# Kernel tuning notes

Hardware: AMD Instinct MI355X
Metric: run time of the kernel (lower is better)

Reference implementation:

```python
import jax, jax.numpy as jnp
import numpy as np

N = 120000   # current nodes
F = 256      # num_feat
H = 256      # num_hidden
L = 64       # num_logits
E_MP = 1000000  # message-passing edges
E = 200000      # scored edges
PREV = [60000, 80000, 100000]
PROX_WEIGHT = 0.3


def setup_inputs() -> dict:
    key = jax.random.key(0)
    ks = jax.random.split(key, 40)
    n = lambda k, shape, s=0.05: jax.random.normal(k, shape, dtype=jnp.float32) * s
    inp = {}
    inp["x"] = n(ks[0], (N, F), 1.0)
    inp["mp_adj"] = jax.random.randint(ks[1], (2, E_MP), 0, N)
    inp["edges"] = jax.random.randint(ks[2], (2, E), 0, N)
    inp["index"] = jax.random.randint(ks[3], (E,), 0, E)
    inp["prev_emb0"] = n(ks[4], (PREV[0], H), 1.0)
    inp["prev_emb1"] = n(ks[5], (PREV[1], H), 1.0)
    inp["prev_emb2"] = n(ks[6], (PREV[2], H), 1.0)
    # Module_L params
    inp["gc1_W"] = n(ks[7], (F, H))
    inp["gc1_b"] = jnp.zeros((H,), jnp.float32)
    inp["gc2_W"] = n(ks[8], (H, H))
    inp["gc2_b"] = jnp.zeros((H,), jnp.float32)
    inp["linear_W"] = n(ks[9], (2 * H, H))
    inp["linear_b"] = jnp.zeros((H,), jnp.float32)
    inp["weight_lin"] = n(ks[10], (H, H))
    inp["bias_lin"] = jnp.zeros((H,), jnp.float32)
    inp["w_q"] = n(ks[11], (H, H))
    inp["w_k"] = n(ks[12], (H, H))
    inp["w_v"] = n(ks[13], (H, H))
    # ensemble params
    inp["ml_w1"] = n(ks[14], (2 * H, H)); inp["ml_b1"] = jnp.zeros((H,), jnp.float32)
    inp["ml_w2"] = n(ks[15], (H, 1));     inp["ml_b2"] = jnp.zeros((1,), jnp.float32)
    inp["ms_w1"] = n(ks[16], (2 * H, H)); inp["ms_b1"] = jnp.zeros((H,), jnp.float32)
    inp["ms_w2"] = n(ks[17], (H, 1));     inp["ms_b2"] = jnp.zeros((1,), jnp.float32)
    inp["msdr_w"] = n(ks[18], (L, H));    inp["msdr_b"] = jnp.zeros((H,), jnp.float32)
    # Module_S logits and precomputed score tables
    inp["logits"] = n(ks[19], (N, L), 1.0)
    inp["ms_train_score"] = jax.random.uniform(ks[20], (E,), dtype=jnp.float32)
    inp["prox_train_score"] = jax.random.uniform(ks[21], (E,), dtype=jnp.float32)
    return inp


def _gcn(x, W, b, src, dst, n_nodes):
    xw = x @ W
    loop = jnp.arange(n_nodes)
    s = jnp.concatenate([src, loop])
    d = jnp.concatenate([dst, loop])
    deg = jax.ops.segment_sum(jnp.ones_like(d, dtype=xw.dtype), d, num_segments=n_nodes)
    dinv = jax.lax.rsqrt(jnp.maximum(deg, 1.0))
    norm = (dinv[s] * dinv[d])[:, None]
    out = jax.ops.segment_sum(xw[s] * norm, d, num_segments=n_nodes)
    return out + b


def _mean_max(a, b):
    return jnp.concatenate([(a + b) * 0.5, jnp.maximum(a, b)], axis=1)


def reference(x, mp_adj, edges, index, prev_emb0, prev_emb1, prev_emb2,
              gc1_W, gc1_b, gc2_W, gc2_b, linear_W, linear_b,
              weight_lin, bias_lin, w_q, w_k, w_v,
              ml_w1, ml_b1, ml_w2, ml_b2, ms_w1, ms_b1, ms_w2, ms_b2,
              msdr_w, msdr_b, logits, ms_train_score, prox_train_score):
    src_mp, dst_mp = mp_adj[0], mp_adj[1]
    # --- Module_L: 2-layer GCN encoder (dropout = identity in eval) ---
    h = jnp.tanh(_gcn(x, gc1_W, gc1_b, src_mp, dst_mp, N))
    emb = jnp.tanh(_gcn(h, gc2_W, gc2_b, src_mp, dst_mp, N))

    # --- ragged per-window temporal attention over previous snapshots ---
    prev = [prev_emb0, prev_emb1, prev_emb2]
    T = len(prev)
    start = 0
    parts = []
    for i in range(T):
        end = prev[i].shape[0]
        if end == N:
            break
        # stack snapshots i..T-1 plus current, restricted to window [start:end)
        stack = jnp.stack([prev[j][start:end] for j in range(i, T)] + [emb[start:end]], axis=0)  # [S,n,H]
        q = emb[start:end] @ w_q              # [n,H]
        k = stack @ w_k                        # [S,n,H]
        v = stack @ w_v                        # [S,n,H]
        attn = jnp.einsum('nh,snh->ns', q, k) / np.sqrt(np.float32(H))
        w = jax.nn.softmax(attn, axis=-1)      # [n,S]
        parts.append(jnp.einsum('ns,snh->nh', w, v))
        start = end
    if start != N:
        parts.append(emb[start:] @ w_v)
    attn_emb = jnp.concatenate(parts, axis=0)  # [N,H]

    emb2 = jnp.tanh(jnp.concatenate([emb, attn_emb], axis=1) @ linear_W + linear_b)  # [N,H]

    # --- symmetric bilinear edge scores ---
    sym = (weight_lin + weight_lin.T) * 0.5
    es, ed = edges[0], edges[1]
    sim = ((emb2[es] @ sym) * emb2[ed] + bias_lin).sum(axis=1)
    ml_scores = jax.nn.sigmoid(sim)            # [E]

    # --- Module_S / Proximity: table lookups ---
    ms_scores = ms_train_score[index]
    prox_scores = prox_train_score[index]

    # --- ensemble weighted sum ---
    scores = jnp.stack([ml_scores, ms_scores, prox_scores], axis=1)  # [E,3]
    ml_feat = _mean_max(emb2[es], emb2[ed])                          # [E,2H]
    a_ml = jnp.tanh(jnp.tanh(ml_feat @ ml_w1 + ml_b1) @ ml_w2 + ml_b2)
    r0 = jnp.tanh(logits[es] @ msdr_w + msdr_b)
    r1 = jnp.tanh(logits[ed] @ msdr_w + msdr_b)
    a_ms = jnp.tanh(jnp.tanh(_mean_max(r0, r1) @ ms_w1 + ms_b1) @ ms_w2 + ms_b2)
    a_px = jnp.full_like(a_ml, PROX_WEIGHT)
    attn_w = jax.nn.softmax(jnp.concatenate([a_ml, a_ms, a_px], axis=1), axis=1)  # [E,3]
    final = jnp.clip((scores * attn_w).sum(axis=1), 0.0, 1.0)
    return final
```

## Files before the change

kernel.cpp:

```cpp
#include <hip/hip_runtime.h>
#include <hip/hip_bf16.h>

#define Nn_   120000
#define F_    256
#define H_    256
#define L_    64
#define EMP_  1000000
#define E_    200000
#define P0_   60000
#define P1_   80000
#define P2_   100000
#define PROXW 0.3f

typedef __attribute__((ext_vector_type(8))) short bf16x8;
typedef __attribute__((ext_vector_type(4))) float f32x4;

__device__ inline float bf2f(unsigned short u) {
    union { unsigned int i; float f; } x; x.i = ((unsigned int)u) << 16; return x.f;
}
__device__ inline unsigned short f2bf(float f) {
    union { float f; unsigned int i; } x; x.f = f;
    unsigned int r = x.i + 0x7fffu + ((x.i >> 16) & 1u);
    return (unsigned short)(r >> 16);
}
__device__ inline float tanh_fast(float x) {
    float e = __expf(2.0f * x);
    return 1.0f - 2.0f * __builtin_amdgcn_rcpf(e + 1.0f);
}
__device__ inline float sigmoid_fast(float z) {
    return __builtin_amdgcn_rcpf(1.0f + __expf(-z));
}
__device__ inline int lds_off(int row, int s) {
    return row * 64 + ((s ^ ((row >> 1) & 3)) << 4);
}
__device__ inline void gload_lds16(const void* g, void* l) {
    __builtin_amdgcn_global_load_lds((const __attribute__((address_space(1))) void*)g,
                                     (__attribute__((address_space(3))) void*)l, 16, 0, 0);
}
__device__ inline void unpk8(uint4 u, float* o) {
    o[0] = bf2f(u.x & 0xffff); o[1] = bf2f(u.x >> 16);
    o[2] = bf2f(u.y & 0xffff); o[3] = bf2f(u.y >> 16);
    o[4] = bf2f(u.z & 0xffff); o[5] = bf2f(u.z >> 16);
    o[6] = bf2f(u.w & 0xffff); o[7] = bf2f(u.w >> 16);
}
__device__ inline void meanmax_u(unsigned int ua, unsigned int ub,
                                 unsigned int& um, unsigned int& ux) {
    float alo = __uint_as_float(ua << 16);
    float ahi = __uint_as_float(ua & 0xffff0000u);
    float blo = __uint_as_float(ub << 16);
    float bhi = __uint_as_float(ub & 0xffff0000u);
    um = (unsigned int)f2bf((alo + blo) * 0.5f) |
         ((unsigned int)f2bf((ahi + bhi) * 0.5f) << 16);
    ux = (__float_as_uint(fmaxf(alo, blo)) >> 16) |
         (__float_as_uint(fmaxf(ahi, bhi)) & 0xffff0000u);
}
__device__ inline float dot2_u(unsigned int ug, unsigned int ub) {
    float gl = __uint_as_float(ug << 16);
    float gh = __uint_as_float(ug & 0xffff0000u);
    float bl = __uint_as_float(ub << 16);
    float bh = __uint_as_float(ub & 0xffff0000u);
    return fmaf(gl, bl, gh * bh);
}

__global__ void k_count(const int* __restrict__ dst, int* __restrict__ cnt, int n) {
    int e = blockIdx.x * 256 + threadIdx.x;
    if (e < n) atomicAdd(&cnt[dst[e]], 1);
}
__global__ void k_block_reduce(const int* __restrict__ cnt, int* __restrict__ bsum, int n) {
    __shared__ int s[256];
    int i = blockIdx.x * 256 + threadIdx.x;
    s[threadIdx.x] = (i < n) ? cnt[i] : 0;
    __syncthreads();
    for (int o = 128; o > 0; o >>= 1) {
        if (threadIdx.x < o) s[threadIdx.x] += s[threadIdx.x + o];
        __syncthreads();
    }
    if (threadIdx.x == 0) bsum[blockIdx.x] = s[0];
}
__global__ void k_scan_bsum(int* bsum, int nb) {
    if (threadIdx.x == 0 && blockIdx.x == 0) {
        int acc = 0;
        for (int i = 0; i < nb; i++) { int v = bsum[i]; bsum[i] = acc; acc += v; }
    }
}
__global__ void k_scan_final(const int* __restrict__ cnt, const int* __restrict__ bsum,
                             int* __restrict__ rowp, int n, int etot) {
    __shared__ int s[256];
    int tid = threadIdx.x;
    int i = blockIdx.x * 256 + tid;
    int v = (i < n) ? cnt[i] : 0;
    s[tid] = v;
    __syncthreads();
    for (int o = 1; o < 256; o <<= 1) {
        int t = 0;
        if (tid >= o) t = s[tid - o];
        __syncthreads();
        s[tid] += t;
        __syncthreads();
    }
    if (i < n) rowp[i] = bsum[blockIdx.x] + s[tid] - v;
    if (i == 0 && blockIdx.x == 0) rowp[n] = etot;
}
__global__ void k_fill(const int* __restrict__ src, const int* __restrict__ dst,
                       const int* __restrict__ rowp, int* __restrict__ fill,
                       int* __restrict__ csr, int n) {
    int e = blockIdx.x * 256 + threadIdx.x;
    if (e < n) {
        int d = dst[e];
        int p = atomicAdd(&fill[d], 1);
        csr[rowp[d] + p] = src[e];
    }
}
__global__ void k_dinv(const int* __restrict__ cnt, float* __restrict__ dinv, int n) {
    int i = blockIdx.x * 256 + threadIdx.x;
    if (i < n) dinv[i] = rsqrtf((float)cnt[i] + 1.0f);
}

#define TM 64
#define TN 64
#define TK 16
template <bool TRANSB>
__global__ void gemm_tiled(const float* __restrict__ A, const float* __restrict__ B,
                           float* __restrict__ C, int M, int K, int N) {
    __shared__ float As[TK][TM + 4];
    __shared__ float Bs[TK][TN + 4];
    int tid = threadIdx.x;
    int tx = tid & 15, ty = tid >> 4;
    int row0 = blockIdx.y * TM, col0 = blockIdx.x * TN;
    int lr = tid >> 2, lc4 = (tid & 3) * 4;
    float acc[4][4] = {};
    for (int k0 = 0; k0 < K; k0 += TK) {
        {
            int gr = row0 + lr;
            float4 v = make_float4(0.f, 0.f, 0.f, 0.f);
            if (gr < M) v = *(const float4*)(A + (size_t)gr * K + k0 + lc4);
            As[lc4 + 0][lr] = v.x; As[lc4 + 1][lr] = v.y;
            As[lc4 + 2][lr] = v.z; As[lc4 + 3][lr] = v.w;
        }
        {
            int n = tid & 63, kk0 = tid >> 6;
#pragma unroll
            for (int p = 0; p < 4; p++) {
                int kk = kk0 + p * 4;
                if (TRANSB) Bs[kk][n] = B[(size_t)(col0 + n) * K + k0 + kk];
                else        Bs[kk][n] = B[(size_t)(k0 + kk) * N + col0 + n];
            }
        }
        __syncthreads();
#pragma unroll
        for (int kk = 0; kk < TK; kk++) {
            float4 a = *(const float4*)&As[kk][ty * 4];
            float4 b = *(const float4*)&Bs[kk][tx * 4];
            float av[4] = {a.x, a.y, a.z, a.w};
            float bv[4] = {b.x, b.y, b.z, b.w};
#pragma unroll
            for (int i = 0; i < 4; i++)
#pragma unroll
                for (int j = 0; j < 4; j++) acc[i][j] += av[i] * bv[j];
        }
        __syncthreads();
    }
#pragma unroll
    for (int i = 0; i < 4; i++) {
        int r = row0 + ty * 4 + i;
        if (r >= M) continue;
#pragma unroll
        for (int j = 0; j < 4; j++) C[(size_t)r * N + col0 + tx * 4 + j] = acc[i][j];
    }
}

__global__ void k_cvt(const float* __restrict__ in, unsigned short* __restrict__ out, int n4) {
    int i = blockIdx.x * 256 + threadIdx.x;
    if (i >= n4) return;
    float4 v = ((const float4*)in)[i];
    ushort4 o;
    o.x = f2bf(v.x); o.y = f2bf(v.y); o.z = f2bf(v.z); o.w = f2bf(v.w);
    ((ushort4*)out)[i] = o;
}

__device__ inline void packBF_task(const float* __restrict__ Wsrc,
                                   unsigned short* __restrict__ P, int blk) {
    int t = blk * 256 + threadIdx.x;
    int c = t >> 6, l = t & 63;
    int os = c >> 5, half = (c >> 4) & 1, colb = c & 15;
    int col = (colb << 4) + (l & 15);
    int k = (half << 8) + (os << 5) + ((l >> 4) << 3);
    bf16x8 v;
#pragma unroll
    for (int j = 0; j < 8; ++j) v[j] = (short)f2bf(Wsrc[(size_t)(k + j) * 256 + col]);
    *(bf16x8*)(P + (size_t)t * 8) = v;
}

__global__ void k_prep1(const float* __restrict__ gc1W, const float* __restrict__ gc2W,
                        const float* __restrict__ msdrW, const float* __restrict__ wlin,
                        const float* __restrict__ blin, const float* __restrict__ mlw1,
                        const float* __restrict__ msw1,
                        unsigned short* __restrict__ gc1Wt, unsigned short* __restrict__ gc2Wt,
                        unsigned short* __restrict__ msdrWt, unsigned short* __restrict__ symb,
                        float* __restrict__ sumb, unsigned short* __restrict__ mlPk,
                        unsigned short* __restrict__ msPk) {
    __shared__ float s[256];
    int b = blockIdx.x, tid = threadIdx.x;
    if (b < 256) {
        int c = b;
        for (int r = tid; r < 256; r += 256) gc1Wt[c * 256 + r] = f2bf(gc1W[(size_t)r * 256 + c]);
    } else if (b < 512) {
        int c = b - 256;
        for (int r = tid; r < 256; r += 256) gc2Wt[c * 256 + r] = f2bf(gc2W[(size_t)r * 256 + c]);
    } else if (b < 768) {
        int c = b - 512;
        if (tid < 64) msdrWt[c * 64 + tid] = f2bf(msdrW[(size_t)tid * 256 + c]);
    } else if (b < 1024) {
        int r = b - 768, c = tid;
        symb[r * 256 + c] = f2bf(0.5f * (wlin[r * 256 + c] + wlin[c * 256 + r]));
    } else if (b == 1024) {
        s[tid] = blin[tid];
        __syncthreads();
        for (int o = 128; o > 0; o >>= 1) {
            if (tid < o) s[tid] += s[tid + o];
            __syncthreads();
        }
        if (tid == 0) sumb[0] = s[0];
    } else if (b < 1089) {
        packBF_task(mlw1, mlPk, b - 1025);
    } else {
        packBF_task(msw1, msPk, b - 1089);
    }
}
__global__ void k_prep2(const float* __restrict__ Mqk, const float* __restrict__ linW,
                        const float* __restrict__ W2w, unsigned short* __restrict__ MqkT,
                        unsigned short* __restrict__ Bt) {
    int b = blockIdx.x, tid = threadIdx.x;
    if (b < 256) {
        int c = b;
        for (int r = tid; r < 256; r += 256) MqkT[c * 256 + r] = f2bf(Mqk[(size_t)r * 256 + c]);
    } else {
        int idx = (b - 256) * 256 + tid;
        int n = idx >> 9, k = idx & 511;
        float v = (k < 256) ? linW[(size_t)k * 256 + n] : W2w[(size_t)(k - 256) * 256 + n];
        Bt[idx] = f2bf(v);
    }
}

__global__ __launch_bounds__(256)
void k_agg_bf(const unsigned short* __restrict__ xw, const int* __restrict__ rowp,
              const int* __restrict__ csr, const float* __restrict__ dinv,
              const float* __restrict__ bias, unsigned short* __restrict__ out) {
    int w = threadIdx.x >> 6, lane = threadIdx.x & 63;
    int v = blockIdx.x * 4 + w;
    if (v >= Nn_) return;
    const uint2* x64 = (const uint2*)xw;
    float a0 = 0.f, a1 = 0.f, a2 = 0.f, a3 = 0.f;
    int beg = rowp[v], end = rowp[v + 1];
    uint2 un = make_uint2(0, 0); float dn = 0.f;
    if (beg < end) {
        int s0 = csr[beg];
        dn = dinv[s0];
        un = x64[(size_t)s0 * 64 + lane];
    }
    for (int p = beg; p < end; ++p) {
        uint2 uc = un; float dc = dn;
        if (p + 1 < end) {
            int s1 = csr[p + 1];
            dn = dinv[s1];
            un = x64[(size_t)s1 * 64 + lane];
        }
        a0 += bf2f(uc.x & 0xffff) * dc;
        a1 += bf2f(uc.x >> 16) * dc;
        a2 += bf2f(uc.y & 0xffff) * dc;
        a3 += bf2f(uc.y >> 16) * dc;
    }
    float dv = dinv[v];
    uint2 us = x64[(size_t)v * 64 + lane];
    a0 = a0 * dv + bf2f(us.x & 0xffff) * dv * dv;
    a1 = a1 * dv + bf2f(us.x >> 16) * dv * dv;
    a2 = a2 * dv + bf2f(us.y & 0xffff) * dv * dv;
    a3 = a3 * dv + bf2f(us.y >> 16) * dv * dv;
    int c0 = lane * 4;
    float4 bv = *(const float4*)(bias + c0);
    uint2 ov;
    ov.x = (unsigned int)f2bf(tanh_fast(a0 + bv.x)) |
           ((unsigned int)f2bf(tanh_fast(a1 + bv.y)) << 16);
    ov.y = (unsigned int)f2bf(tanh_fast(a2 + bv.z)) |
           ((unsigned int)f2bf(tanh_fast(a3 + bv.w)) << 16);
    ((uint2*)out)[(size_t)v * 64 + lane] = ov;
}

template <bool BIAS, bool TANH>
__global__ __launch_bounds__(256)
void mfma_gemm(const unsigned short* __restrict__ A0, const unsigned short* __restrict__ A1,
               int Ksplit, int K, const unsigned short* __restrict__ Bt,
               const float* __restrict__ bias, unsigned short* __restrict__ Cb, int M) {
    __shared__ char lds[2][16384];
    int tid = threadIdx.x, lane = tid & 63, w = tid >> 6;
    int row0 = blockIdx.y * 128, col0 = blockIdx.x * 128;
    int wr = w >> 1, wc = w & 1;
    f32x4 acc[4][4] = {};
    int nk = K >> 5;

    auto stage = [&](int ks, int buf) {
        int k0 = ks << 5;
        #pragma unroll
        for (int j = 0; j < 4; ++j) {
            int ins = w + (j << 2);
            int lrow = ((ins & 7) << 4) + (lane >> 2);
            int p = lane & 3;
            int slog = p ^ ((lrow >> 1) & 3);
            char* ldst = lds[buf] + ((ins & 7) << 10) + ((ins >= 8) ? 8192 : 0);
            const unsigned short* src;
            if (ins < 8) {
                int grow = row0 + lrow;
                if (grow >= M) grow = M - 1;
                const unsigned short* Asrc; int kk, pitch;
                if (k0 < Ksplit) { Asrc = A0; kk = k0; pitch = Ksplit; }
                else             { Asrc = A1; kk = k0 - Ksplit; pitch = K - Ksplit; }
                src = Asrc + (size_t)grow * pitch + kk + (slog << 3);
            } else {
                int grow = col0 + lrow;
                src = Bt + (size_t)grow * K + k0 + (slog << 3);
            }
            gload_lds16(src, ldst);
        }
    };

    stage(0, 0);
    for (int ks = 0; ks < nk; ++ks) {
        int cur = ks & 1;
        if (ks + 1 < nk) {
            stage(ks + 1, cur ^ 1);
            asm volatile("s_waitcnt vmcnt(4)" ::: "memory");
        } else {
            asm volatile("s_waitcnt vmcnt(0)" ::: "memory");
        }
        __builtin_amdgcn_s_barrier();
        __builtin_amdgcn_sched_barrier(0);
        int s = lane >> 4, r16 = lane & 15;
        bf16x8 a[4], b[4];
        #pragma unroll
        for (int m = 0; m < 4; ++m) a[m] = *(const bf16x8*)(lds[cur] + lds_off(wr * 64 + m * 16 + r16, s));
        #pragma unroll
        for (int n = 0; n < 4; ++n) b[n] = *(const bf16x8*)(lds[cur] + 8192 + lds_off(wc * 64 + n * 16 + r16, s));
        __builtin_amdgcn_s_setprio(1);
        #pragma unroll
        for (int m = 0; m < 4; ++m)
            #pragma unroll
            for (int n = 0; n < 4; ++n)
                acc[m][n] = __builtin_amdgcn_mfma_f32_16x16x32_bf16(a[m], b[n], acc[m][n], 0, 0, 0);
        __builtin_amdgcn_s_setprio(0);
        __builtin_amdgcn_s_barrier();
        __builtin_amdgcn_sched_barrier(0);
    }
    int q = lane >> 4, r16 = lane & 15;
    float bv[4];
    #pragma unroll
    for (int n = 0; n < 4; ++n) bv[n] = BIAS ? bias[col0 + wc * 64 + n * 16 + r16] : 0.f;
    #pragma unroll
    for (int m = 0; m < 4; ++m) {
        #pragma unroll
        for (int i = 0; i < 4; ++i) {
            int row = row0 + wr * 64 + m * 16 + q * 4 + i;
            if (row >= M) continue;
            #pragma unroll
            for (int n = 0; n < 4; ++n) {
                int col = col0 + wc * 64 + n * 16 + r16;
                float v = acc[m][n][i];
                if (BIAS) v += bv[n];
                if (TANH) v = tanh_fast(v);
                Cb[(size_t)row * 256 + col] = f2bf(v);
            }
        }
    }
}

__global__ __launch_bounds__(256)
void k_attn_u2(const unsigned short* __restrict__ emb, const unsigned short* __restrict__ t,
               const float* __restrict__ p0, const float* __restrict__ p1,
               const float* __restrict__ p2, unsigned short* __restrict__ u) {
    int tid = threadIdx.x;
    int g = tid >> 4, l = tid & 15;
    int n = blockIdx.x * 16 + g;
    size_t eoff = (size_t)n * 256 + l * 16;
    const uint4* e16 = (const uint4*)(emb + eoff);
    uint4* u16 = (uint4*)(u + eoff);
    uint4 eb0 = e16[0], eb1 = e16[1];
    if (n >= P2_) { u16[0] = eb0; u16[1] = eb1; return; }
    float tv[16], ev[16];
    {
        const uint4* t16 = (const uint4*)(t + eoff);
        unpk8(t16[0], tv); unpk8(t16[1], tv + 8);
        unpk8(eb0, ev); unpk8(eb1, ev + 8);
    }
    float m = -3.0e38f, den = 0.f, o[16];
    #pragma unroll
    for (int i = 0; i < 16; i++) o[i] = 0.f;
    auto accum = [&](const float* sv) {
        float dt = 0.f;
        #pragma unroll
        for (int i = 0; i < 16; i++) dt += tv[i] * sv[i];
        dt += __shfl_xor(dt, 1);
        dt += __shfl_xor(dt, 2);
        dt += __shfl_xor(dt, 4);
        dt += __shfl_xor(dt, 8);
        float lg = dt * 0.0625f;
        float mn = fmaxf(m, lg);
        float s0 = __expf(m - mn), s1 = __expf(lg - mn);
        den = den * s0 + s1;
        #pragma unroll
        for (int i = 0; i < 16; i++) o[i] = o[i] * s0 + s1 * sv[i];
        m = mn;
    };
    auto accum_f32 = [&](const float* base) {
        float sv[16];
        const float4* b4 = (const float4*)(base + eoff);
        #pragma unroll
        for (int i = 0; i < 4; i++) {
            float4 q = b4[i];
            sv[4 * i] = q.x; sv[4 * i + 1] = q.y; sv[4 * i + 2] = q.z; sv[4 * i + 3] = q.w;
        }
        accum(sv);
    };
    if (n < P0_)      { accum_f32(p0); accum_f32(p1); accum_f32(p2); }
    else if (n < P1_) { accum_f32(p1); accum_f32(p2); }
    else              { accum_f32(p2); }
    accum(ev);
    float inv = __builtin_amdgcn_rcpf(den);
    unsigned short h[16];
    #pragma unroll
    for (int i = 0; i < 16; i++) h[i] = f2bf(o[i] * inv);
    uint4 r0, r1;
    r0.x = h[0] | ((unsigned int)h[1] << 16);  r0.y = h[2] | ((unsigned int)h[3] << 16);
    r0.z = h[4] | ((unsigned int)h[5] << 16);  r0.w = h[6] | ((unsigned int)h[7] << 16);
    r1.x = h[8] | ((unsigned int)h[9] << 16);  r1.y = h[10] | ((unsigned int)h[11] << 16);
    r1.z = h[12] | ((unsigned int)h[13] << 16); r1.w = h[14] | ((unsigned int)h[15] << 16);
    u16[0] = r0; u16[1] = r1;
}

template <bool SIM>
__global__ __launch_bounds__(256)
void mfma_edge4(const unsigned short* __restrict__ srcemb, const unsigned short* __restrict__ gsrc,
                const int* __restrict__ es, const int* __restrict__ ed,
                const unsigned short* __restrict__ PkF, const float* __restrict__ b1,
                const float* __restrict__ w2, const float* __restrict__ sumb,
                float* __restrict__ a_pre, float* __restrict__ mlsc) {
    __shared__ char lds[8192];
    __shared__ float red[64];
    int tid = threadIdx.x, lane = tid & 63, w = tid >> 6;
    int e0 = blockIdx.x * 64;
    int arow = tid >> 2, p = tid & 3;
    int ia = es[e0 + arow], ib = ed[e0 + arow];
    const unsigned short* ra = srcemb + (size_t)ia * 256;
    const unsigned short* rb = srcemb + (size_t)ib * 256;
    const unsigned short* rg = SIM ? (gsrc + (size_t)ia * 256) : nullptr;
    int slog = p ^ ((arow >> 1) & 3);
    int co = slog << 3;
    int abase = arow * 64 + (p << 4);
    if (tid < 64) red[tid] = 0.f;
    f32x4 acc[4][4] = {};
    float simacc = 0.f;
    const bf16x8* BF = (const bf16x8*)PkF;
    uint4 pa0 = *(const uint4*)(ra + co);
    uint4 pb0 = *(const uint4*)(rb + co);
    uint4 pa1 = *(const uint4*)(ra + 32 + co);
    uint4 pb1 = *(const uint4*)(rb + 32 + co);
    uint4 pa2 = *(const uint4*)(ra + 64 + co);
    uint4 pb2 = *(const uint4*)(rb + 64 + co);
    uint4 pa3 = *(const uint4*)(ra + 96 + co);
    uint4 pb3 = *(const uint4*)(rb + 96 + co);
    uint4 pg0 = make_uint4(0, 0, 0, 0), pg1 = pg0, pg2 = pg0, pg3 = pg0;
    if (SIM) {
        pg0 = *(const uint4*)(rg + co);
        pg1 = *(const uint4*)(rg + 32 + co);
        pg2 = *(const uint4*)(rg + 64 + co);
        pg3 = *(const uint4*)(rg + 96 + co);
    }
    #pragma unroll
    for (int os = 0; os < 8; ++os) {
        uint4 ua = pa0, ub = pb0, ug = pg0;
        pa0 = pa1; pa1 = pa2; pa2 = pa3;
        pb0 = pb1; pb1 = pb2; pb2 = pb3;
        if (SIM) { pg0 = pg1; pg1 = pg2; pg2 = pg3; }
        if (os < 4) {
            int cb = ((os + 4) << 5) + co;
            pa3 = *(const uint4*)(ra + cb);
            pb3 = *(const uint4*)(rb + cb);
            if (SIM) pg3 = *(const uint4*)(rg + cb);
        }
        {
            unsigned int m0, x0, m1, x1, m2, x2, m3, x3;
            meanmax_u(ua.x, ub.x, m0, x0);
            meanmax_u(ua.y, ub.y, m1, x1);
            meanmax_u(ua.z, ub.z, m2, x2);
            meanmax_u(ua.w, ub.w, m3, x3);
            *(uint4*)(lds + abase) = make_uint4(m0, m1, m2, m3);
            *(uint4*)(lds + 4096 + abase) = make_uint4(x0, x1, x2, x3);
            if (SIM)
                simacc += dot2_u(ug.x, ub.x) + dot2_u(ug.y, ub.y) +
                          dot2_u(ug.z, ub.z) + dot2_u(ug.w, ub.w);
        }
        asm volatile("s_waitcnt lgkmcnt(0)" ::: "memory");
        __builtin_amdgcn_s_barrier();
        __builtin_amdgcn_sched_barrier(0);
        int s = lane >> 4, r16 = lane & 15;
        {
            bf16x8 b0[4], a[4];
            #pragma unroll
            for (int n2 = 0; n2 < 4; ++n2)
                b0[n2] = BF[(size_t)((((os << 1) << 4) + (w << 2) + n2) * 64 + lane)];
            #pragma unroll
            for (int m2 = 0; m2 < 4; ++m2)
                a[m2] = *(const bf16x8*)(lds + lds_off(m2 * 16 + r16, s));
            __builtin_amdgcn_s_setprio(1);
            #pragma unroll
            for (int m2 = 0; m2 < 4; ++m2)
                #pragma unroll
                for (int n2 = 0; n2 < 4; ++n2)
                    acc[m2][n2] = __builtin_amdgcn_mfma_f32_16x16x32_bf16(a[m2], b0[n2], acc[m2][n2], 0, 0, 0);
            __builtin_amdgcn_s_setprio(0);
        }
        {
            bf16x8 b1r[4], a[4];
            #pragma unroll
            for (int n2 = 0; n2 < 4; ++n2)
                b1r[n2] = BF[(size_t)(((((os << 1) + 1) << 4) + (w << 2) + n2) * 64 + lane)];
            #pragma unroll
            for (int m2 = 0; m2 < 4; ++m2)
                a[m2] = *(const bf16x8*)(lds + 4096 + lds_off(m2 * 16 + r16, s));
            __builtin_amdgcn_s_setprio(1);
            #pragma unroll
            for (int m2 = 0; m2 < 4; ++m2)
                #pragma unroll
                for (int n2 = 0; n2 < 4; ++n2)
                    acc[m2][n2] = __builtin_amdgcn_mfma_f32_16x16x32_bf16(a[m2], b1r[n2], acc[m2][n2], 0, 0, 0);
            __builtin_amdgcn_s_setprio(0);
        }
        __builtin_amdgcn_s_barrier();
        __builtin_amdgcn_sched_barrier(0);
    }
    int q = lane >> 4, r16 = lane & 15;
    float b1c[4], w2c[4];
    #pragma unroll
    for (int n2 = 0; n2 < 4; ++n2) {
        int c = (w << 6) + n2 * 16 + r16;
        b1c[n2] = b1[c]; w2c[n2] = w2[c];
    }
    #pragma unroll
    for (int m2 = 0; m2 < 4; ++m2) {
        #pragma unroll
        for (int i = 0; i < 4; ++i) {
            int row = m2 * 16 + q * 4 + i;
            float ps = 0.f;
            #pragma unroll
            for (int n2 = 0; n2 < 4; ++n2) ps += tanh_fast(acc[m2][n2][i] + b1c[n2]) * w2c[n2];
            ps += __shfl_xor(ps, 1);
            ps += __shfl_xor(ps, 2);
            ps += __shfl_xor(ps, 4);
            ps += __shfl_xor(ps, 8);
            if (r16 == 0) atomicAdd(&red[row], ps);
        }
    }
    if (SIM) {
        simacc += __shfl_xor(simacc, 1);
        simacc += __shfl_xor(simacc, 2);
        if (p == 0) mlsc[e0 + arow] = sigmoid_fast(simacc + sumb[0]);
    }
    __syncthreads();
    if (tid < 64) a_pre[e0 + tid] = red[tid];
}

__global__ void k_final(const float* __restrict__ apml, const float* __restrict__ apms,
                        const float* __restrict__ mlsc, const float* __restrict__ mstr,
                        const float* __restrict__ pxtr, const int* __restrict__ index,
                        const float* __restrict__ mlb2, const float* __restrict__ msb2,
                        float* __restrict__ out) {
    int e = blockIdx.x * 256 + threadIdx.x;
    if (e >= E_) return;
    float aml = tanh_fast(apml[e] + mlb2[0]);
    float ams = tanh_fast(apms[e] + msb2[0]);
    float apx = PROXW;
    float m = fmaxf(aml, fmaxf(ams, apx));
    float wml = __expf(aml - m), wms = __expf(ams - m), wpx = __expf(apx - m);
    float inv = __builtin_amdgcn_rcpf(wml + wms + wpx);
    int idx = index[e];
    float v = (mlsc[e] * wml + mstr[idx] * wms + pxtr[idx] * wpx) * inv;
    out[e] = fminf(fmaxf(v, 0.f), 1.f);
}

__global__ void k_sentinel(float* out, int n) {
    int i = blockIdx.x * 256 + threadIdx.x;
    if (i < n) out[i] = -12345.0f;
}

extern "C" void kernel_launch(void* const* d_in, const int* in_sizes, int n_in,
                              void* d_out, int out_size, void* d_ws, size_t ws_size,
                              hipStream_t stream) {
    const float* x     = (const float*)d_in[0];
    const int*   mp    = (const int*)d_in[1];
    const int*   edges = (const int*)d_in[2];
    const int*   index = (const int*)d_in[3];
    const float* p0    = (const float*)d_in[4];
    const float* p1    = (const float*)d_in[5];
    const float* p2    = (const float*)d_in[6];
    const float* gc1W  = (const float*)d_in[7];
    const float* gc1b  = (const float*)d_in[8];
    const float* gc2W  = (const float*)d_in[9];
    const float* gc2b  = (const float*)d_in[10];
    const float* linW  = (const float*)d_in[11];
    const float* linb  = (const float*)d_in[12];
    const float* wlin  = (const float*)d_in[13];
    const float* blin  = (const float*)d_in[14];
    const float* wq    = (const float*)d_in[15];
    const float* wk    = (const float*)d_in[16];
    const float* wv    = (const float*)d_in[17];
    const float* mlw1  = (const float*)d_in[18];
    const float* mlb1  = (const float*)d_in[19];
    const float* mlw2  = (const float*)d_in[20];
    const float* mlb2  = (const float*)d_in[21];
    const float* msw1  = (const float*)d_in[22];
    const float* msb1  = (const float*)d_in[23];
    const float* msw2  = (const float*)d_in[24];
    const float* msb2  = (const float*)d_in[25];
    const float* msdrW = (const float*)d_in[26];
    const float* msdrb = (const float*)d_in[27];
    const float* logits = (const float*)d_in[28];
    const float* mstr  = (const float*)d_in[29];
    const float* pxtr  = (const float*)d_in[30];
    float* out = (float*)d_out;

    const int* src_mp = mp;
    const int* dst_mp = mp + EMP_;
    const int* es = edges;
    const int* ed = edges + E_;

    char* ws = (char*)d_ws;
    size_t off = 0;
    auto alloc = [&](size_t bytes) -> char* {
        off = (off + 255) & ~(size_t)255;
        char* r = ws + off;
        off += bytes;
        return r;
    };
    const size_t NODE_BF = (size_t)Nn_ * 256 * 2;
    unsigned short* W0 = (unsigned short*)alloc(NODE_BF);
    unsigned short* W1 = (unsigned short*)alloc(NODE_BF);
    unsigned short* W2 = (unsigned short*)alloc(NODE_BF);
    unsigned short* W3 = (unsigned short*)alloc(NODE_BF);
    unsigned short* W4 = (unsigned short*)alloc(NODE_BF);
    unsigned short* W5 = (unsigned short*)alloc(NODE_BF);
    int*   cnt  = (int*)alloc((size_t)Nn_ * 4);
    int*   rowp = (int*)alloc((size_t)(Nn_ + 1) * 4);
    int*   fill = (int*)alloc((size_t)Nn_ * 4);
    int*   csr  = (int*)alloc((size_t)EMP_ * 4);
    float* dinv = (float*)alloc((size_t)Nn_ * 4);
    int*   bsum = (int*)alloc(512 * 4);
    float* Mqk  = (float*)alloc(65536 * 4);
    float* W2wf = (float*)alloc(65536 * 4);
    unsigned short* gc1Wt = (unsigned short*)alloc(65536 * 2);
    unsigned short* gc2Wt = (unsigned short*)alloc(65536 * 2);
    unsigned short* MqkT  = (unsigned short*)alloc(65536 * 2);
    unsigned short* Bt512 = (unsigned short*)alloc(131072 * 2);
    unsigned short* symb  = (unsigned short*)alloc(65536 * 2);
    unsigned short* msdrWt = (unsigned short*)alloc(16384 * 2);
    unsigned short* mlPk  = (unsigned short*)alloc(131072 * 2);
    unsigned short* msPk  = (unsigned short*)alloc(131072 * 2);
    float* apml = (float*)alloc((size_t)E_ * 4);
    float* apms = (float*)alloc((size_t)E_ * 4);
    float* mlsc = (float*)alloc((size_t)E_ * 4);
    float* sumb = (float*)alloc(256);

    if (off > ws_size) {
        k_sentinel<<<(E_ + 255) / 256, 256, 0, stream>>>(out, E_);
        return;
    }

    hipMemsetAsync(cnt, 0, (size_t)Nn_ * 4, stream);
    hipMemsetAsync(fill, 0, (size_t)Nn_ * 4, stream);

    const int NB = (Nn_ + 255) / 256;
    const int EB = (EMP_ + 255) / 256;

    k_cvt<<<30000, 256, 0, stream>>>(x, W0, Nn_ * 256 / 4);
    k_prep1<<<1153, 256, 0, stream>>>(gc1W, gc2W, msdrW, wlin, blin, mlw1, msw1,
                                      gc1Wt, gc2Wt, msdrWt, symb, sumb, mlPk, msPk);
    dim3 gSmall(4, 4);
    gemm_tiled<true><<<gSmall, 256, 0, stream>>>(wq, wk, Mqk, 256, 256, 256);
    gemm_tiled<false><<<gSmall, 256, 0, stream>>>(wv, linW + 256 * 256, W2wf, 256, 256, 256);
    k_prep2<<<768, 256, 0, stream>>>(Mqk, linW, W2wf, MqkT, Bt512);

    k_count<<<EB, 256, 0, stream>>>(dst_mp, cnt, EMP_);
    k_block_reduce<<<NB, 256, 0, stream>>>(cnt, bsum, Nn_);
    k_scan_bsum<<<1, 64, 0, stream>>>(bsum, NB);
    k_scan_final<<<NB, 256, 0, stream>>>(cnt, bsum, rowp, Nn_, EMP_);
    k_fill<<<EB, 256, 0, stream>>>(src_mp, dst_mp, rowp, fill, csr, EMP_);
    k_dinv<<<NB, 256, 0, stream>>>(cnt, dinv, Nn_);

    dim3 gFull(2, (Nn_ + 127) / 128);
    dim3 gT(2, (P2_ + 127) / 128);
    const int AGG_B = (Nn_ + 3) / 4;

    mfma_gemm<false, false><<<gFull, 256, 0, stream>>>(W0, W0, 256, 256, gc1Wt, nullptr, W1, Nn_);
    k_agg_bf<<<AGG_B, 256, 0, stream>>>(W1, rowp, csr, dinv, gc1b, W2);
    mfma_gemm<false, false><<<gFull, 256, 0, stream>>>(W2, W2, 256, 256, gc2Wt, nullptr, W1, Nn_);
    k_agg_bf<<<AGG_B, 256, 0, stream>>>(W1, rowp, csr, dinv, gc2b, W3);

    mfma_gemm<false, false><<<gT, 256, 0, stream>>>(W3, W3, 256, 256, MqkT, nullptr, W4, P2_);
    k_attn_u2<<<Nn_ / 16, 256, 0, stream>>>(W3, W4, p0, p1, p2, W4);

    mfma_gemm<true, true><<<gFull, 256, 0, stream>>>(W3, W4, 256, 512, Bt512, linb, W5, Nn_);

    mfma_gemm<false, false><<<gFull, 256, 0, stream>>>(W5, W5, 256, 256, symb, nullptr, W0, Nn_);

    k_cvt<<<7500, 256, 0, stream>>>(logits, W1, Nn_ * 64 / 4);
    mfma_gemm<true, true><<<gFull, 256, 0, stream>>>(W1, W1, 64, 64, msdrWt, msdrb, W2, Nn_);

    mfma_edge4<true><<<E_ / 64, 256, 0, stream>>>(W5, W0, es, ed, mlPk, mlb1, mlw2, sumb, apml, mlsc);
    mfma_edge4<false><<<E_ / 64, 256, 0, stream>>>(W2, nullptr, es, ed, msPk, msb1, msw2, sumb, apms, nullptr);

    k_final<<<(E_ + 255) / 256, 256, 0, stream>>>(apml, apms, mlsc, mstr, pxtr, index, mlb2, msb2, out);
}
```

Baseline: 1.028 ms.

## Stage gathered edge embedding rows into LDS via direct global-to-LDS loads

The edge MLP kernel now gathers all 64 source and 64 destination embedding rows for a block into a 64 KB LDS buffer up front, using direct global-to-LDS loads with an XOR swizzle. This replaces the per-thread register prefetch pipeline that interleaved global loads with the mean/max and MFMA stages. The similarity dot product is now computed once from LDS before the GEMM loop instead of being spread across it. The goal is fully coalesced, wide row gathers and fewer live registers, at the cost of much larger LDS per block, which lowers occupancy and serializes the gather ahead of compute.

New measurement: 1.057 ms. 2.9% more time.

```diff
diff --git a/kernel.cpp b/kernel.cpp
--- a/kernel.cpp
+++ b/kernel.cpp
@@ -437,65 +437,68 @@
 
 template <bool SIM>
 __global__ __launch_bounds__(256)
-void mfma_edge4(const unsigned short* __restrict__ srcemb, const unsigned short* __restrict__ gsrc,
+void mfma_edge5(const unsigned short* __restrict__ srcemb, const unsigned short* __restrict__ gsrc,
                 const int* __restrict__ es, const int* __restrict__ ed,
                 const unsigned short* __restrict__ PkF, const float* __restrict__ b1,
                 const float* __restrict__ w2, const float* __restrict__ sumb,
                 float* __restrict__ a_pre, float* __restrict__ mlsc) {
-    __shared__ char lds[8192];
+    __shared__ char lds[65536 + 8192];
     __shared__ float red[64];
     int tid = threadIdx.x, lane = tid & 63, w = tid >> 6;
     int e0 = blockIdx.x * 64;
     int arow = tid >> 2, p = tid & 3;
-    int ia = es[e0 + arow], ib = ed[e0 + arow];
-    const unsigned short* ra = srcemb + (size_t)ia * 256;
-    const unsigned short* rb = srcemb + (size_t)ib * 256;
-    const unsigned short* rg = SIM ? (gsrc + (size_t)ia * 256) : nullptr;
-    int slog = p ^ ((arow >> 1) & 3);
-    int co = slog << 3;
-    int abase = arow * 64 + (p << 4);
+    uint4 greg[8];
+    if (SIM) {
+        int ia_own = es[e0 + arow];
+        const unsigned short* rg = gsrc + (size_t)ia_own * 256 + (p << 6);
+        #pragma unroll
+        for (int j = 0; j < 8; ++j) greg[j] = *(const uint4*)(rg + (j << 3));
+    }
+    {
+        int half = lane >> 5, l5 = lane & 31;
+        #pragma unroll 4
+        for (int j = 0; j < 16; ++j) {
+            int q = (w << 4) + j;
+            int node = (half ? ed : es)[e0 + q];
+            int cg = l5 ^ (q & 7);
+            const unsigned short* src = srcemb + (size_t)node * 256 + (cg << 3);
+            gload_lds16(src, lds + (q << 10));
+        }
+    }
     if (tid < 64) red[tid] = 0.f;
+    asm volatile("s_waitcnt vmcnt(0)" ::: "memory");
+    __builtin_amdgcn_s_barrier();
+    if (SIM) {
+        float simacc = 0.f;
+        #pragma unroll
+        for (int j = 0; j < 8; ++j) {
+            int k = (p << 3) + j;
+            int c = k ^ (arow & 7);
+            uint4 bb = *(const uint4*)(lds + (arow << 10) + 512 + (c << 4));
+            simacc += dot2_u(greg[j].x, bb.x) + dot2_u(greg[j].y, bb.y) +
+                      dot2_u(greg[j].z, bb.z) + dot2_u(greg[j].w, bb.w);
+        }
+        simacc += __shfl_xor(simacc, 1);
+        simacc += __shfl_xor(simacc, 2);
+        if (p == 0) mlsc[e0 + arow] = sigmoid_fast(simacc + sumb[0]);
+    }
     f32x4 acc[4][4] = {};
-    float simacc = 0.f;
     const bf16x8* BF = (const bf16x8*)PkF;
-    uint4 pa0 = *(const uint4*)(ra + co);
-    uint4 pb0 = *(const uint4*)(rb + co);
-    uint4 pa1 = *(const uint4*)(ra + 32 + co);
-    uint4 pb1 = *(const uint4*)(rb + 32 + co);
-    uint4 pa2 = *(const uint4*)(ra + 64 + co);
-    uint4 pb2 = *(const uint4*)(rb + 64 + co);
-    uint4 pa3 = *(const uint4*)(ra + 96 + co);
-    uint4 pb3 = *(const uint4*)(rb + 96 + co);
-    uint4 pg0 = make_uint4(0, 0, 0, 0), pg1 = pg0, pg2 = pg0, pg3 = pg0;
-    if (SIM) {
-        pg0 = *(const uint4*)(rg + co);
-        pg1 = *(const uint4*)(rg + 32 + co);
-        pg2 = *(const uint4*)(rg + 64 + co);
-        pg3 = *(const uint4*)(rg + 96 + co);
-    }
-    #pragma unroll
+    int swA = p ^ ((arow >> 1) & 3);
+    const int AT = 65536;
     for (int os = 0; os < 8; ++os) {
-        uint4 ua = pa0, ub = pb0, ug = pg0;
-        pa0 = pa1; pa1 = pa2; pa2 = pa3;
-        pb0 = pb1; pb1 = pb2; pb2 = pb3;
-        if (SIM) { pg0 = pg1; pg1 = pg2; pg2 = pg3; }
-        if (os < 4) {
-            int cb = ((os + 4) << 5) + co;
-            pa3 = *(const uint4*)(ra + cb);
-            pb3 = *(const uint4*)(rb + cb);
-            if (SIM) pg3 = *(const uint4*)(rg + cb);
-        }
         {
+            int k = (os << 2) + p;
+            int c = k ^ (arow & 7);
+            uint4 ua = *(const uint4*)(lds + (arow << 10) + (c << 4));
+            uint4 ub = *(const uint4*)(lds + (arow << 10) + 512 + (c << 4));
             unsigned int m0, x0, m1, x1, m2, x2, m3, x3;
             meanmax_u(ua.x, ub.x, m0, x0);
             meanmax_u(ua.y, ub.y, m1, x1);
             meanmax_u(ua.z, ub.z, m2, x2);
             meanmax_u(ua.w, ub.w, m3, x3);
-            *(uint4*)(lds + abase) = make_uint4(m0, m1, m2, m3);
-            *(uint4*)(lds + 4096 + abase) = make_uint4(x0, x1, x2, x3);
-            if (SIM)
-                simacc += dot2_u(ug.x, ub.x) + dot2_u(ug.y, ub.y) +
-                          dot2_u(ug.z, ub.z) + dot2_u(ug.w, ub.w);
+            *(uint4*)(lds + AT + arow * 64 + (swA << 4)) = make_uint4(m0, m1, m2, m3);
+            *(uint4*)(lds + AT + 4096 + arow * 64 + (swA << 4)) = make_uint4(x0, x1, x2, x3);
         }
         asm volatile("s_waitcnt lgkmcnt(0)" ::: "memory");
         __builtin_amdgcn_s_barrier();
@@ -508,7 +511,7 @@
                 b0[n2] = BF[(size_t)((((os << 1) << 4) + (w << 2) + n2) * 64 + lane)];
             #pragma unroll
             for (int m2 = 0; m2 < 4; ++m2)
-                a[m2] = *(const bf16x8*)(lds + lds_off(m2 * 16 + r16, s));
+                a[m2] = *(const bf16x8*)(lds + AT + lds_off(m2 * 16 + r16, s));
             __builtin_amdgcn_s_setprio(1);
             #pragma unroll
             for (int m2 = 0; m2 < 4; ++m2)
@@ -524,7 +527,7 @@
                 b1r[n2] = BF[(size_t)(((((os << 1) + 1) << 4) + (w << 2) + n2) * 64 + lane)];
             #pragma unroll
             for (int m2 = 0; m2 < 4; ++m2)
-                a[m2] = *(const bf16x8*)(lds + 4096 + lds_off(m2 * 16 + r16, s));
+                a[m2] = *(const bf16x8*)(lds + AT + 4096 + lds_off(m2 * 16 + r16, s));
             __builtin_amdgcn_s_setprio(1);
             #pragma unroll
             for (int m2 = 0; m2 < 4; ++m2)
@@ -557,11 +560,6 @@
             ps += __shfl_xor(ps, 8);
             if (r16 == 0) atomicAdd(&red[row], ps);
         }
-    }
-    if (SIM) {
-        simacc += __shfl_xor(simacc, 1);
-        simacc += __shfl_xor(simacc, 2);
-        if (p == 0) mlsc[e0 + arow] = sigmoid_fast(simacc + sumb[0]);
     }
     __syncthreads();
     if (tid < 64) a_pre[e0 + tid] = red[tid];
@@ -712,8 +710,8 @@
     k_cvt<<<7500, 256, 0, stream>>>(logits, W1, Nn_ * 64 / 4);
     mfma_gemm<true, true><<<gFull, 256, 0, stream>>>(W1, W1, 64, 64, msdrWt, msdrb, W2, Nn_);
 
-    mfma_edge4<true><<<E_ / 64, 256, 0, stream>>>(W5, W0, es, ed, mlPk, mlb1, mlw2, sumb, apml, mlsc);
-    mfma_edge4<false><<<E_ / 64, 256, 0, stream>>>(W2, nullptr, es, ed, msPk, msb1, msw2, sumb, apms, nullptr);
+    mfma_edge5<true><<<E_ / 64, 256, 0, stream>>>(W5, W0, es, ed, mlPk, mlb1, mlw2, sumb, apml, mlsc);
+    mfma_edge5<false><<<E_ / 64, 256, 0, stream>>>(W2, nullptr, es, ed, msPk, msb1, msw2, sumb, apms, nullptr);
 
     k_final<<<(E_ + 255) / 256, 256, 0, stream>>>(apml, apms, mlsc, mstr, pxtr, index, mlb2, msb2, out);
 }
```

## Fuse ML and MS edge MLP kernels into one dual-accumulator edge kernel

Applied to the files above, without the earlier changes.

Merges the two per-edge mean/max MLP kernels (ML branch on emb2 and MS branch on the logits projection) into a single kernel that gathers both tables for each edge tile and runs both MFMA chains with separate accumulators. This removes one launch and the second read of the edge index arrays, and lets the two gathers overlap. The 4-deep register prefetch pipeline is replaced by a 1-deep prefetch, and the kernel now holds doubled accumulators and LDS (16KB). That raises register pressure and may lower occupancy and latency hiding.

Result: slower. 1.109 ms (+7.9%).

```diff
diff --git a/kernel.cpp b/kernel.cpp
--- a/kernel.cpp
+++ b/kernel.cpp
@@ -435,136 +435,170 @@
     u16[0] = r0; u16[1] = r1;
 }
 
-template <bool SIM>
 __global__ __launch_bounds__(256)
-void mfma_edge4(const unsigned short* __restrict__ srcemb, const unsigned short* __restrict__ gsrc,
+void mfma_edge6(const unsigned short* __restrict__ emb2, const unsigned short* __restrict__ rtab,
+                const unsigned short* __restrict__ gsrc,
                 const int* __restrict__ es, const int* __restrict__ ed,
-                const unsigned short* __restrict__ PkF, const float* __restrict__ b1,
-                const float* __restrict__ w2, const float* __restrict__ sumb,
-                float* __restrict__ a_pre, float* __restrict__ mlsc) {
-    __shared__ char lds[8192];
-    __shared__ float red[64];
+                const unsigned short* __restrict__ PkMl, const unsigned short* __restrict__ PkMs,
+                const float* __restrict__ b1ml, const float* __restrict__ w2ml,
+                const float* __restrict__ b1ms, const float* __restrict__ w2ms,
+                const float* __restrict__ sumb,
+                float* __restrict__ apml, float* __restrict__ apms,
+                float* __restrict__ mlsc) {
+    __shared__ char lds[16384];
+    __shared__ float redml[64], redms[64];
     int tid = threadIdx.x, lane = tid & 63, w = tid >> 6;
     int e0 = blockIdx.x * 64;
     int arow = tid >> 2, p = tid & 3;
     int ia = es[e0 + arow], ib = ed[e0 + arow];
-    const unsigned short* ra = srcemb + (size_t)ia * 256;
-    const unsigned short* rb = srcemb + (size_t)ib * 256;
-    const unsigned short* rg = SIM ? (gsrc + (size_t)ia * 256) : nullptr;
+    const unsigned short* ea = emb2 + (size_t)ia * 256;
+    const unsigned short* eb = emb2 + (size_t)ib * 256;
+    const unsigned short* ra = rtab + (size_t)ia * 256;
+    const unsigned short* rb = rtab + (size_t)ib * 256;
+    const unsigned short* rg = gsrc + (size_t)ia * 256;
     int slog = p ^ ((arow >> 1) & 3);
     int co = slog << 3;
     int abase = arow * 64 + (p << 4);
-    if (tid < 64) red[tid] = 0.f;
-    f32x4 acc[4][4] = {};
+    if (tid < 64) { redml[tid] = 0.f; redms[tid] = 0.f; }
+    f32x4 accml[4][4] = {}, accms[4][4] = {};
     float simacc = 0.f;
-    const bf16x8* BF = (const bf16x8*)PkF;
-    uint4 pa0 = *(const uint4*)(ra + co);
-    uint4 pb0 = *(const uint4*)(rb + co);
-    uint4 pa1 = *(const uint4*)(ra + 32 + co);
-    uint4 pb1 = *(const uint4*)(rb + 32 + co);
-    uint4 pa2 = *(const uint4*)(ra + 64 + co);
-    uint4 pb2 = *(const uint4*)(rb + 64 + co);
-    uint4 pa3 = *(const uint4*)(ra + 96 + co);
-    uint4 pb3 = *(const uint4*)(rb + 96 + co);
-    uint4 pg0 = make_uint4(0, 0, 0, 0), pg1 = pg0, pg2 = pg0, pg3 = pg0;
-    if (SIM) {
-        pg0 = *(const uint4*)(rg + co);
-        pg1 = *(const uint4*)(rg + 32 + co);
-        pg2 = *(const uint4*)(rg + 64 + co);
-        pg3 = *(const uint4*)(rg + 96 + co);
-    }
-    #pragma unroll
+    const bf16x8* BL = (const bf16x8*)PkMl;
+    const bf16x8* BS = (const bf16x8*)PkMs;
+    uint4 pea = *(const uint4*)(ea + co);
+    uint4 peb = *(const uint4*)(eb + co);
+    uint4 pra = *(const uint4*)(ra + co);
+    uint4 prb = *(const uint4*)(rb + co);
+    uint4 pg  = *(const uint4*)(rg + co);
     for (int os = 0; os < 8; ++os) {
-        uint4 ua = pa0, ub = pb0, ug = pg0;
-        pa0 = pa1; pa1 = pa2; pa2 = pa3;
-        pb0 = pb1; pb1 = pb2; pb2 = pb3;
-        if (SIM) { pg0 = pg1; pg1 = pg2; pg2 = pg3; }
-        if (os < 4) {
-            int cb = ((os + 4) << 5) + co;
-            pa3 = *(const uint4*)(ra + cb);
-            pb3 = *(const uint4*)(rb + cb);
-            if (SIM) pg3 = *(const uint4*)(rg + cb);
-        }
         {
             unsigned int m0, x0, m1, x1, m2, x2, m3, x3;
-            meanmax_u(ua.x, ub.x, m0, x0);
-            meanmax_u(ua.y, ub.y, m1, x1);
-            meanmax_u(ua.z, ub.z, m2, x2);
-            meanmax_u(ua.w, ub.w, m3, x3);
+            meanmax_u(pea.x, peb.x, m0, x0); meanmax_u(pea.y, peb.y, m1, x1);
+            meanmax_u(pea.z, peb.z, m2, x2); meanmax_u(pea.w, peb.w, m3, x3);
             *(uint4*)(lds + abase) = make_uint4(m0, m1, m2, m3);
             *(uint4*)(lds + 4096 + abase) = make_uint4(x0, x1, x2, x3);
-            if (SIM)
-                simacc += dot2_u(ug.x, ub.x) + dot2_u(ug.y, ub.y) +
-                          dot2_u(ug.z, ub.z) + dot2_u(ug.w, ub.w);
+            simacc += dot2_u(pg.x, peb.x) + dot2_u(pg.y, peb.y) +
+                      dot2_u(pg.z, peb.z) + dot2_u(pg.w, peb.w);
+            meanmax_u(pra.x, prb.x, m0, x0); meanmax_u(pra.y, prb.y, m1, x1);
+            meanmax_u(pra.z, prb.z, m2, x2); meanmax_u(pra.w, prb.w, m3, x3);
+            *(uint4*)(lds + 8192 + abase) = make_uint4(m0, m1, m2, m3);
+            *(uint4*)(lds + 12288 + abase) = make_uint4(x0, x1, x2, x3);
+        }
+        bf16x8 bml0[4], bml1[4], bms0[4], bms1[4];
+        #pragma unroll
+        for (int n2 = 0; n2 < 4; ++n2) {
+            int c0i = (os << 5) + (w << 2) + n2;
+            bml0[n2] = BL[(size_t)c0i * 64 + lane];
+            bml1[n2] = BL[(size_t)(c0i + 16) * 64 + lane];
+            bms0[n2] = BS[(size_t)c0i * 64 + lane];
+            bms1[n2] = BS[(size_t)(c0i + 16) * 64 + lane];
+        }
+        if (os < 7) {
+            int cb = ((os + 1) << 5) + co;
+            pea = *(const uint4*)(ea + cb);
+            peb = *(const uint4*)(eb + cb);
+            pra = *(const uint4*)(ra + cb);
+            prb = *(const uint4*)(rb + cb);
+            pg  = *(const uint4*)(rg + cb);
         }
         asm volatile("s_waitcnt lgkmcnt(0)" ::: "memory");
         __builtin_amdgcn_s_barrier();
         __builtin_amdgcn_sched_barrier(0);
         int s = lane >> 4, r16 = lane & 15;
-        {
-            bf16x8 b0[4], a[4];
+        bf16x8 a[4];
+        #pragma unroll
+        for (int m2 = 0; m2 < 4; ++m2) a[m2] = *(const bf16x8*)(lds + lds_off(m2 * 16 + r16, s));
+        __builtin_amdgcn_s_setprio(1);
+        #pragma unroll
+        for (int m2 = 0; m2 < 4; ++m2)
             #pragma unroll
             for (int n2 = 0; n2 < 4; ++n2)
-                b0[n2] = BF[(size_t)((((os << 1) << 4) + (w << 2) + n2) * 64 + lane)];
-            #pragma unroll
-            for (int m2 = 0; m2 < 4; ++m2)
-                a[m2] = *(const bf16x8*)(lds + lds_off(m2 * 16 + r16, s));
-            __builtin_amdgcn_s_setprio(1);
-            #pragma unroll
-            for (int m2 = 0; m2 < 4; ++m2)
-                #pragma unroll
-                for (int n2 = 0; n2 < 4; ++n2)
-                    acc[m2][n2] = __builtin_amdgcn_mfma_f32_16x16x32_bf16(a[m2], b0[n2], acc[m2][n2], 0, 0, 0);
-            __builtin_amdgcn_s_setprio(0);
-        }
-        {
-            bf16x8 b1r[4], a[4];
+                accml[m2][n2] = __builtin_amdgcn_mfma_f32_16x16x32_bf16(a[m2], bml0[n2], accml[m2][n2], 0, 0, 0);
+        __builtin_amdgcn_s_setprio(0);
+        #pragma unroll
+        for (int m2 = 0; m2 < 4; ++m2) a[m2] = *(const bf16x8*)(lds + 4096 + lds_off(m2 * 16 + r16, s));
+        __builtin_amdgcn_s_setprio(1);
+        #pragma unroll
+        for (int m2 = 0; m2 < 4; ++m2)
             #pragma unroll
             for (int n2 = 0; n2 < 4; ++n2)
-                b1r[n2] = BF[(size_t)(((((os << 1) + 1) << 4) + (w << 2) + n2) * 64 + lane)];
+                accml[m2][n2] = __builtin_amdgcn_mfma_f32_16x16x32_bf16(a[m2], bml1[n2], accml[m2][n2], 0, 0, 0);
+        __builtin_amdgcn_s_setprio(0);
+        #pragma unroll
+        for (int m2 = 0; m2 < 4; ++m2) a[m2] = *(const bf16x8*)(lds + 8192 + lds_off(m2 * 16 + r16, s));
+        __builtin_amdgcn_s_setprio(1);
+        #pragma unroll
+        for (int m2 = 0; m2 < 4; ++m2)
             #pragma unroll
-            for (int m2 = 0; m2 < 4; ++m2)
-                a[m2] = *(const bf16x8*)(lds + 4096 + lds_off(m2 * 16 + r16, s));
-            __builtin_amdgcn_s_setprio(1);
+            for (int n2 = 0; n2 < 4; ++n2)
+                accms[m2][n2] = __builtin_amdgcn_mfma_f32_16x16x32_bf16(a[m2], bms0[n2], accms[m2][n2], 0, 0, 0);
+        __builtin_amdgcn_s_setprio(0);
+        #pragma unroll
+        for (int m2 = 0; m2 < 4; ++m2) a[m2] = *(const bf16x8*)(lds + 12288 + lds_off(m2 * 16 + r16, s));
+        __builtin_amdgcn_s_setprio(1);
+        #pragma unroll
+        for (int m2 = 0; m2 < 4; ++m2)
             #pragma unroll
-            for (int m2 = 0; m2 < 4; ++m2)
-                #pragma unroll
-                for (int n2 = 0; n2 < 4; ++n2)
-                    acc[m2][n2] = __builtin_amdgcn_mfma_f32_16x16x32_bf16(a[m2], b1r[n2], acc[m2][n2], 0, 0, 0);
-            __builtin_amdgcn_s_setprio(0);
-        }
+            for (int n2 = 0; n2 < 4; ++n2)
+                accms[m2][n2] = __builtin_amdgcn_mfma_f32_16x16x32_bf16(a[m2], bms1[n2], accms[m2][n2], 0, 0, 0);
+        __builtin_amdgcn_s_setprio(0);
         __builtin_amdgcn_s_barrier();
         __builtin_amdgcn_sched_barrier(0);
     }
     int q = lane >> 4, r16 = lane & 15;
-    float b1c[4], w2c[4];
-    #pragma unroll
-    for (int n2 = 0; n2 < 4; ++n2) {
-        int c = (w << 6) + n2 * 16 + r16;
-        b1c[n2] = b1[c]; w2c[n2] = w2[c];
-    }
-    #pragma unroll
-    for (int m2 = 0; m2 < 4; ++m2) {
-        #pragma unroll
-        for (int i = 0; i < 4; ++i) {
-            int row = m2 * 16 + q * 4 + i;
-            float ps = 0.f;
+    {
+        float b1c[4], w2c[4];
+        #pragma unroll
+        for (int n2 = 0; n2 < 4; ++n2) {
+            int c = (w << 6) + n2 * 16 + r16;
+            b1c[n2] = b1ml[c]; w2c[n2] = w2ml[c];
+        }
+        #pragma unroll
+        for (int m2 = 0; m2 < 4; ++m2) {
             #pragma unroll
-            for (int n2 = 0; n2 < 4; ++n2) ps += tanh_fast(acc[m2][n2][i] + b1c[n2]) * w2c[n2];
-            ps += __shfl_xor(ps, 1);
-            ps += __shfl_xor(ps, 2);
-            ps += __shfl_xor(ps, 4);
-            ps += __shfl_xor(ps, 8);
-            if (r16 == 0) atomicAdd(&red[row], ps);
-        }
-    }
-    if (SIM) {
-        simacc += __shfl_xor(simacc, 1);
-        simacc += __shfl_xor(simacc, 2);
-        if (p == 0) mlsc[e0 + arow] = sigmoid_fast(simacc + sumb[0]);
-    }
+            for (int i = 0; i < 4; ++i) {
+                int row = m2 * 16 + q * 4 + i;
+                float ps = 0.f;
+                #pragma unroll
+                for (int n2 = 0; n2 < 4; ++n2) ps += tanh_fast(accml[m2][n2][i] + b1c[n2]) * w2c[n2];
+                ps += __shfl_xor(ps, 1);
+                ps += __shfl_xor(ps, 2);
+                ps += __shfl_xor(ps, 4);
+                ps += __shfl_xor(ps, 8);
+                if (r16 == 0) atomicAdd(&redml[row], ps);
+            }
+        }
+    }
+    {
+        float b1c[4], w2c[4];
+        #pragma unroll
+        for (int n2 = 0; n2 < 4; ++n2) {
+            int c = (w << 6) + n2 * 16 + r16;
+            b1c[n2] = b1ms[c]; w2c[n2] = w2ms[c];
+        }
+        #pragma unroll
+        for (int m2 = 0; m2 < 4; ++m2) {
+            #pragma unroll
+            for (int i = 0; i < 4; ++i) {
+                int row = m2 * 16 + q * 4 + i;
+                float ps = 0.f;
+                #pragma unroll
+                for (int n2 = 0; n2 < 4; ++n2) ps += tanh_fast(accms[m2][n2][i] + b1c[n2]) * w2c[n2];
+                ps += __shfl_xor(ps, 1);
+                ps += __shfl_xor(ps, 2);
+                ps += __shfl_xor(ps, 4);
+                ps += __shfl_xor(ps, 8);
+                if (r16 == 0) atomicAdd(&redms[row], ps);
+            }
+        }
+    }
+    simacc += __shfl_xor(simacc, 1);
+    simacc += __shfl_xor(simacc, 2);
+    if (p == 0) mlsc[e0 + arow] = sigmoid_fast(simacc + sumb[0]);
     __syncthreads();
-    if (tid < 64) a_pre[e0 + tid] = red[tid];
+    if (tid < 64) {
+        apml[e0 + tid] = redml[tid];
+        apms[e0 + tid] = redms[tid];
+    }
 }
 
 __global__ void k_final(const float* __restrict__ apml, const float* __restrict__ apms,
@@ -712,8 +746,8 @@
     k_cvt<<<7500, 256, 0, stream>>>(logits, W1, Nn_ * 64 / 4);
     mfma_gemm<true, true><<<gFull, 256, 0, stream>>>(W1, W1, 64, 64, msdrWt, msdrb, W2, Nn_);
 
-    mfma_edge4<true><<<E_ / 64, 256, 0, stream>>>(W5, W0, es, ed, mlPk, mlb1, mlw2, sumb, apml, mlsc);
-    mfma_edge4<false><<<E_ / 64, 256, 0, stream>>>(W2, nullptr, es, ed, msPk, msb1, msw2, sumb, apms, nullptr);
+    mfma_edge6<<<E_ / 64, 256, 0, stream>>>(W5, W2, W0, es, ed, mlPk, msPk,
+                                            mlb1, mlw2, msb1, msw2, sumb, apml, apms, mlsc);
 
     k_final<<<(E_ + 255) / 256, 256, 0, stream>>>(apml, apms, mlsc, mstr, pxtr, index, mlb2, msb2, out);
 }
```
